# Optimization experiments

Hardware: AMD Instinct MI355X
Metric: run time of the kernel (lower is better)

The kernel has to match this reference:

```python
import jax, jax.numpy as jnp
import numpy as np

D_MODEL = 1024
NUM_HEADS = 16
HEAD_DIM = D_MODEL // NUM_HEADS


def setup_inputs() -> dict:
    key = jax.random.key(0)
    k_x, k_wqkv, k_bqkv, k_wo, k_bo = jax.random.split(key, 5)
    B, T = 2, 2048
    bound_qkv = 1.0 / np.sqrt(D_MODEL)
    bound_o = 1.0 / np.sqrt(D_MODEL)
    return {
        "x": jax.random.normal(k_x, (B, T, D_MODEL), dtype=jnp.float32),
        # stored as (in, out) for clean x @ W
        "w_qkv": jax.random.uniform(k_wqkv, (D_MODEL, 3 * D_MODEL), jnp.float32, -bound_qkv, bound_qkv),
        "b_qkv": jax.random.uniform(k_bqkv, (3 * D_MODEL,), jnp.float32, -bound_qkv, bound_qkv),
        "w_out": jax.random.uniform(k_wo, (D_MODEL, D_MODEL), jnp.float32, -bound_o, bound_o),
        "b_out": jax.random.uniform(k_bo, (D_MODEL,), jnp.float32, -bound_o, bound_o),
    }


def reference(x, w_qkv, b_qkv, w_out, b_out):
    B, T, C = x.shape
    H, Dh = NUM_HEADS, HEAD_DIM
    scale = jnp.sqrt(jnp.asarray(Dh, dtype=x.dtype))
    qkv = x @ w_qkv + b_qkv                      # [B, T, 3C]
    q, k, v = jnp.split(qkv, 3, axis=-1)         # each [B, T, C]
    # [B, T, C] -> [B, H, T, Dh]
    q = q.reshape(B, T, H, Dh).transpose(0, 2, 1, 3)
    k = k.reshape(B, T, H, Dh).transpose(0, 2, 1, 3)
    v = v.reshape(B, T, H, Dh).transpose(0, 2, 1, 3)
    scores = jnp.einsum("bhqd,bhkd->bhqk", q, k) / scale   # [B, H, T, T]
    probs = jax.nn.softmax(scores, axis=-1)
    attn = jnp.einsum("bhqk,bhkd->bhqd", probs, v)          # [B, H, T, Dh]
    attn = attn.transpose(0, 2, 1, 3).reshape(B, T, C)
    return attn @ w_out + b_out
```

## Files before the change

### kernel.cpp

```cpp
#include <hip/hip_runtime.h>
#include <stdint.h>

typedef __bf16 bf16x8 __attribute__((ext_vector_type(8)));
typedef float f32x4 __attribute__((ext_vector_type(4)));
typedef float f32x16 __attribute__((ext_vector_type(16)));
typedef unsigned short u16x8 __attribute__((ext_vector_type(8)));
typedef uint32_t u32x4 __attribute__((ext_vector_type(4)));

#define D_MODEL 1024
#define T_SEQ 2048
#define BATCH 2
#define NHEAD 16
#define HDIM 64
#define MROWS (BATCH * T_SEQ)
#define HEADS_TOTAL (BATCH * NHEAD)
#define QKV_ELEMS (HEADS_TOTAL * T_SEQ * HDIM)

#define QSCALE_LOG2 0.1803368801111204f

__device__ __forceinline__ unsigned short f32_to_bf16_rne(float f) {
    uint32_t u = __builtin_bit_cast(uint32_t, f);
    uint32_t r = (u + 0x7FFFu + ((u >> 16) & 1u)) >> 16;
    return (unsigned short)r;
}

__device__ __forceinline__ uint32_t pack2(float a, float b) {
    return (uint32_t)f32_to_bf16_rne(a) | ((uint32_t)f32_to_bf16_rne(b) << 16);
}

__device__ __forceinline__ void gload_lds16(const void* g, void* l) {
    __builtin_amdgcn_global_load_lds(
        (const __attribute__((address_space(1))) void*)g,
        (__attribute__((address_space(3))) void*)l, 16, 0, 0);
}

__device__ __forceinline__ f32x4 mfma_bf16(bf16x8 a, bf16x8 b, f32x4 c) {
    return __builtin_amdgcn_mfma_f32_16x16x32_bf16(a, b, c, 0, 0, 0);
}
__device__ __forceinline__ f32x16 mfma32(bf16x8 a, bf16x8 b, f32x16 c) {
    return __builtin_amdgcn_mfma_f32_32x32x16_bf16(a, b, c, 0, 0, 0);
}

__global__ void k_convert(const float4* __restrict__ in, u16x8* __restrict__ out, int n8) {
    int i = blockIdx.x * 256 + threadIdx.x;
    if (i >= n8) return;
    float4 a = in[i * 2];
    float4 b = in[i * 2 + 1];
    u16x8 r;
    r[0] = f32_to_bf16_rne(a.x); r[1] = f32_to_bf16_rne(a.y);
    r[2] = f32_to_bf16_rne(a.z); r[3] = f32_to_bf16_rne(a.w);
    r[4] = f32_to_bf16_rne(b.x); r[5] = f32_to_bf16_rne(b.y);
    r[6] = f32_to_bf16_rne(b.z); r[7] = f32_to_bf16_rne(b.w);
    out[i] = r;
}

__global__ void k_transpose_conv(const float* __restrict__ in, unsigned short* __restrict__ out,
                                 int R, int C) {
    __shared__ float tile[32][33];
    int nc = C >> 5;
    int tc0 = (blockIdx.x % nc) * 32;
    int tr0 = (blockIdx.x / nc) * 32;
    int tx = threadIdx.x & 31, ty = threadIdx.x >> 5;
#pragma unroll
    for (int i = 0; i < 4; ++i) {
        int r = ty * 4 + i;
        tile[r][tx] = in[(size_t)(tr0 + r) * C + tc0 + tx];
    }
    __syncthreads();
#pragma unroll
    for (int i = 0; i < 4; ++i) {
        int c = ty * 4 + i;
        out[(size_t)(tc0 + c) * R + tr0 + tx] = f32_to_bf16_rne(tile[tx][c]);
    }
}

template <int EPI>
__global__ __launch_bounds__(256) void k_gemm(const unsigned short* __restrict__ A,
                                              const unsigned short* __restrict__ Bt,
                                              const float* __restrict__ bias,
                                              void* __restrict__ outp,
                                              int M, int N, int K) {
    __shared__ __align__(16) unsigned short As[2][128 * 32];
    __shared__ __align__(16) unsigned short Bs[2][128 * 32];
    const int NB = N >> 7;
    int bm = blockIdx.x / NB, bn = blockIdx.x % NB;
    int tid = threadIdx.x;
    int lane = tid & 63, w = tid >> 6;
    int wr = w >> 1, wc = w & 1;
    int l15 = lane & 15, lg = lane >> 4;

    f32x4 acc[4][4] = {};

    const int nK = K >> 5;
    int c1 = tid, c2 = tid + 256;
    int r1 = c1 >> 2, o1 = (c1 & 3) * 8;
    int r2 = c2 >> 2, o2 = (c2 & 3) * 8;

#define GSTAGE(kt, buf)                                                          \
    do {                                                                         \
        int k0_ = (kt) * 32;                                                     \
        gload_lds16(A + (size_t)(bm * 128 + r1) * K + k0_ + o1,                  \
                    (char*)As[buf] + w * 1024);                                  \
        gload_lds16(A + (size_t)(bm * 128 + r2) * K + k0_ + o2,                  \
                    (char*)As[buf] + 4096 + w * 1024);                           \
        gload_lds16(Bt + (size_t)(bn * 128 + r1) * K + k0_ + o1,                 \
                    (char*)Bs[buf] + w * 1024);                                  \
        gload_lds16(Bt + (size_t)(bn * 128 + r2) * K + k0_ + o2,                 \
                    (char*)Bs[buf] + 4096 + w * 1024);                           \
    } while (0)

    GSTAGE(0, 0);
    __syncthreads();

    for (int kt = 0; kt < nK; ++kt) {
        int cur = kt & 1;
        if (kt + 1 < nK) GSTAGE(kt + 1, cur ^ 1);

        const unsigned short* Ac = As[cur];
        const unsigned short* Bc = Bs[cur];
        bf16x8 af[4], bfr[4];
#pragma unroll
        for (int i = 0; i < 4; ++i)
            af[i] = *(const bf16x8*)(Ac + (wr * 64 + i * 16 + l15) * 32 + lg * 8);
#pragma unroll
        for (int j = 0; j < 4; ++j)
            bfr[j] = *(const bf16x8*)(Bc + (wc * 64 + j * 16 + l15) * 32 + lg * 8);
#pragma unroll
        for (int i = 0; i < 4; ++i)
#pragma unroll
            for (int j = 0; j < 4; ++j)
                acc[i][j] = mfma_bf16(af[i], bfr[j], acc[i][j]);
        __syncthreads();
    }
#undef GSTAGE

    if (EPI == 1) {
        float* out = (float*)outp;
#pragma unroll
        for (int jn = 0; jn < 4; ++jn) {
            int n = bn * 128 + wc * 64 + jn * 16 + l15;
            float bv = bias[n];
#pragma unroll
            for (int i = 0; i < 4; ++i) {
#pragma unroll
                for (int j = 0; j < 4; ++j) {
                    int m = bm * 128 + wr * 64 + i * 16 + lg * 4 + j;
                    out[(size_t)m * N + n] = acc[i][jn][j] + bv;
                }
            }
        }
    } else {
        unsigned short* qkv = (unsigned short*)outp;
#pragma unroll
        for (int jn = 0; jn < 4; ++jn) {
            int n = bn * 128 + wc * 64 + jn * 16 + l15;
            float bv = bias[n];
            int part = n >> 10;
            int cc = n & 1023;
            int h = cc >> 6, d = cc & 63;
            float scale = (part == 0) ? QSCALE_LOG2 : 1.0f;
            unsigned short* dst = qkv + (size_t)part * QKV_ELEMS;
#pragma unroll
            for (int i = 0; i < 4; ++i) {
#pragma unroll
                for (int j = 0; j < 4; ++j) {
                    int m = bm * 128 + wr * 64 + i * 16 + lg * 4 + j;
                    int b = m >> 11, t = m & 2047;
                    float v = (acc[i][jn][j] + bv) * scale;
                    dst[((size_t)(b * NHEAD + h) * T_SEQ + t) * HDIM + d] = f32_to_bf16_rne(v);
                }
            }
        }
    }
}

__global__ void k_transpose_v(const unsigned short* __restrict__ V, unsigned short* __restrict__ Vt) {
    __shared__ unsigned short tile[64][66];
    int bh = blockIdx.x >> 5;
    int t0 = (blockIdx.x & 31) * 64;
    const unsigned short* Vb = V + (size_t)bh * T_SEQ * HDIM;
    unsigned short* Vtb = Vt + (size_t)bh * HDIM * T_SEQ;
    int d = threadIdx.x & 63, tq = threadIdx.x >> 6;
#pragma unroll
    for (int r = 0; r < 16; ++r) {
        int tl = tq * 16 + r;
        tile[tl][d] = Vb[(size_t)(t0 + tl) * HDIM + d];
    }
    __syncthreads();
    int tl = threadIdx.x & 63, dq = threadIdx.x >> 6;
#pragma unroll
    for (int r = 0; r < 16; ++r) {
        int dd = dq * 16 + r;
        Vtb[(size_t)dd * T_SEQ + t0 + tl] = tile[tl][dd];
    }
}

__global__ __launch_bounds__(256) void k_attn(const unsigned short* __restrict__ Qg,
                                              const unsigned short* __restrict__ Kg,
                                              const unsigned short* __restrict__ Vtg,
                                              unsigned short* __restrict__ Og) {
    __shared__ __align__(16) unsigned short Ks[2][64 * 64];
    __shared__ __align__(16) unsigned short Vs[2][64 * 64];

    const int NT = T_SEQ / 64;
    int bid = blockIdx.x;
    int idx = bid >> 3;
    int bh = (bid & 7) * 4 + (idx >> 4);
    int qt = idx & 15;
    int tid = threadIdx.x;
    int w = tid >> 6, lane = tid & 63;
    int l31 = lane & 31, hi = lane >> 5;
    int r7 = l31 & 7;

    const unsigned short* Qb = Qg + (size_t)bh * T_SEQ * HDIM;
    const unsigned short* Kb = Kg + (size_t)bh * T_SEQ * HDIM;
    const unsigned short* Vb = Vtg + (size_t)bh * HDIM * T_SEQ;

    int q0 = qt * 128 + w * 32;

    bf16x8 qf[4];
#pragma unroll
    for (int ks = 0; ks < 4; ++ks)
        qf[ks] = *(const bf16x8*)(Qb + (size_t)(q0 + l31) * HDIM + ks * 16 + hi * 8);

    f32x16 o_[2] = {};
    float m = -INFINITY, l = 0.f;

#define STAGE(tile, buf)                                                             \
    do {                                                                             \
        int kv0s = (tile) * 64;                                                      \
        _Pragma("unroll") for (int i_ = 0; i_ < 2; ++i_) {                           \
            int c_ = i_ * 256 + tid;                                                 \
            int row_ = c_ >> 3;                                                      \
            int cs_ = (c_ & 7) ^ (row_ & 7);                                         \
            gload_lds16(Kb + (size_t)(kv0s + row_) * HDIM + cs_ * 8,                 \
                        (char*)Ks[buf] + i_ * 4096 + w * 1024);                      \
            gload_lds16(Vb + (size_t)row_ * T_SEQ + kv0s + cs_ * 8,                  \
                        (char*)Vs[buf] + i_ * 4096 + w * 1024);                      \
        }                                                                            \
    } while (0)

    STAGE(0, 0);
    __syncthreads();

    for (int t = 0; t < NT; ++t) {
        int cur = t & 1;
        if (t + 1 < NT) STAGE(t + 1, cur ^ 1);

        const char* Kt = (const char*)Ks[cur];
        const char* Vt_ = (const char*)Vs[cur];

        f32x16 s_[2] = {};
#pragma unroll
        for (int ti = 0; ti < 2; ++ti) {
            int row = ti * 32 + l31;
#pragma unroll
            for (int ks = 0; ks < 4; ++ks) {
                bf16x8 kf = *(const bf16x8*)(Kt + row * 128 + ((((ks << 1) | hi) ^ r7) << 4));
                s_[ti] = mfma32(kf, qf[ks], s_[ti]);
            }
        }

        float t16[16];
#pragma unroll
        for (int rr = 0; rr < 16; ++rr) t16[rr] = fmaxf(s_[0][rr], s_[1][rr]);
#pragma unroll
        for (int st = 8; st >= 1; st >>= 1)
#pragma unroll
            for (int rr = 0; rr < 8; ++rr)
                if (rr < st) t16[rr] = fmaxf(t16[rr], t16[rr + st]);
        float mx = fmaxf(t16[0], __shfl_xor(t16[0], 32));

        if (__any(mx - m > 8.0f)) {
            float mn = fmaxf(m, mx);
            float sc = __builtin_exp2f(m - mn);
            m = mn;
            l *= sc;
#pragma unroll
            for (int rr = 0; rr < 16; ++rr) {
                o_[0][rr] *= sc;
                o_[1][rr] *= sc;
            }
        }

        float a16[16];
#pragma unroll
        for (int ti = 0; ti < 2; ++ti)
#pragma unroll
            for (int rr = 0; rr < 16; ++rr) s_[ti][rr] = __builtin_exp2f(s_[ti][rr] - m);
#pragma unroll
        for (int rr = 0; rr < 16; ++rr) a16[rr] = s_[0][rr] + s_[1][rr];
#pragma unroll
        for (int st = 8; st >= 1; st >>= 1)
#pragma unroll
            for (int rr = 0; rr < 8; ++rr)
                if (rr < st) a16[rr] += a16[rr + st];
        l += a16[0] + __shfl_xor(a16[0], 32);

        bf16x8 pa[4];
#pragma unroll
        for (int ks = 0; ks < 4; ++ks) {
            int ti = ks >> 1, k1 = ks & 1;
            uint32_t PA = pack2(s_[ti][8 * k1 + 0], s_[ti][8 * k1 + 1]);
            uint32_t PC = pack2(s_[ti][8 * k1 + 2], s_[ti][8 * k1 + 3]);
            uint32_t PB = pack2(s_[ti][8 * k1 + 4], s_[ti][8 * k1 + 5]);
            uint32_t PD = pack2(s_[ti][8 * k1 + 6], s_[ti][8 * k1 + 7]);
            uint32_t u0 = hi ? PA : PB;
            uint32_t u1 = hi ? PC : PD;
            uint32_t x0 = (uint32_t)__shfl_xor((int)u0, 32);
            uint32_t x1 = (uint32_t)__shfl_xor((int)u1, 32);
            u32x4 ww;
            ww[0] = hi ? x0 : PA;
            ww[1] = hi ? x1 : PC;
            ww[2] = hi ? PB : x0;
            ww[3] = hi ? PD : x1;
            pa[ks] = __builtin_bit_cast(bf16x8, ww);
        }

#pragma unroll
        for (int dn = 0; dn < 2; ++dn) {
            int row = dn * 32 + l31;
#pragma unroll
            for (int ks = 0; ks < 4; ++ks) {
                bf16x8 vf = *(const bf16x8*)(Vt_ + row * 128 + ((((ks << 1) | hi) ^ r7) << 4));
                o_[dn] = mfma32(vf, pa[ks], o_[dn]);
            }
        }
        __syncthreads();
    }
#undef STAGE

    float inv = 1.0f / l;
#pragma unroll
    for (int rr = 0; rr < 16; ++rr) {
        o_[0][rr] *= inv;
        o_[1][rr] *= inv;
    }
    char* eB = (char*)Ks + (size_t)w * 4096;
#pragma unroll
    for (int dn = 0; dn < 2; ++dn)
#pragma unroll
        for (int g = 0; g < 4; ++g) {
            uint32_t w0 = pack2(o_[dn][4 * g], o_[dn][4 * g + 1]);
            uint32_t w1 = pack2(o_[dn][4 * g + 2], o_[dn][4 * g + 3]);
            int c16 = (dn * 4 + g) ^ r7;
            *(uint2*)(eB + l31 * 128 + c16 * 16 + hi * 8) = make_uint2(w0, w1);
        }
    asm volatile("s_waitcnt lgkmcnt(0)" ::: "memory");
    int b = bh >> 4, h = bh & 15;
#pragma unroll
    for (int i = 0; i < 4; ++i) {
        int c = i * 64 + lane;
        int row = c >> 3;
        int c16l = c & 7;
        bf16x8 ov = *(const bf16x8*)(eB + row * 128 + ((c16l ^ (row & 7)) << 4));
        *(bf16x8*)(Og + ((size_t)(b * T_SEQ + q0 + row)) * D_MODEL + h * HDIM + c16l * 8) = ov;
    }
}

extern "C" void kernel_launch(void* const* d_in, const int* in_sizes, int n_in,
                              void* d_out, int out_size, void* d_ws, size_t ws_size,
                              hipStream_t stream) {
    const float* x = (const float*)d_in[0];
    const float* w_qkv = (const float*)d_in[1];
    const float* b_qkv = (const float*)d_in[2];
    const float* w_out = (const float*)d_in[3];
    const float* b_out = (const float*)d_in[4];
    float* out = (float*)d_out;
    char* ws = (char*)d_ws;

    unsigned short* x_bf   = (unsigned short*)(ws + 0);
    unsigned short* wqkv_t = (unsigned short*)(ws + 8388608);
    unsigned short* wout_t = (unsigned short*)(ws + 14680064);
    unsigned short* Qb     = (unsigned short*)(ws + 16777216);
    unsigned short* Kb     = (unsigned short*)(ws + 25165824);
    unsigned short* Vb     = (unsigned short*)(ws + 33554432);
    unsigned short* Vt     = x_bf;
    unsigned short* Ob     = Vb;

    k_convert<<<MROWS * D_MODEL / 8 / 256, 256, 0, stream>>>((const float4*)x, (u16x8*)x_bf,
                                                             MROWS * D_MODEL / 8);
    k_transpose_conv<<<(D_MODEL / 32) * (3 * D_MODEL / 32), 256, 0, stream>>>(w_qkv, wqkv_t,
                                                                              D_MODEL, 3 * D_MODEL);
    k_transpose_conv<<<(D_MODEL / 32) * (D_MODEL / 32), 256, 0, stream>>>(w_out, wout_t,
                                                                          D_MODEL, D_MODEL);
    k_gemm<0><<<(MROWS / 128) * (3 * D_MODEL / 128), 256, 0, stream>>>(x_bf, wqkv_t, b_qkv,
                                                                       (void*)Qb, MROWS,
                                                                       3 * D_MODEL, D_MODEL);
    k_transpose_v<<<HEADS_TOTAL * (T_SEQ / 64), 256, 0, stream>>>(Vb, Vt);
    k_attn<<<512, 256, 0, stream>>>(Qb, Kb, Vt, Ob);
    k_gemm<1><<<(MROWS / 128) * (D_MODEL / 128), 256, 0, stream>>>(Ob, wout_t, b_out, (void*)out,
                                                                   MROWS, D_MODEL, D_MODEL);
}
```

Before: 250.8 us.

## Shrink attention blocks to two waves, use hardware exp and MFMA priority hints

Attention blocks now hold two waves covering 64 queries, launched as 1024 blocks instead of 512, and the staging loop is rewritten with incremental pointers. Exponentials use the raw v_exp_f32 instruction, MFMA sections are wrapped in s_setprio, and the row-sum reduction is moved after the PV matmul to overlap with it. The aim is better occupancy and latency hiding, at the cost of each K/V tile being loaded by fewer waves, which raises global/L2 traffic per query.

```diff
diff --git a/kernel.cpp b/kernel.cpp
--- a/kernel.cpp
+++ b/kernel.cpp
@@ -26,6 +26,12 @@
 
 __device__ __forceinline__ uint32_t pack2(float a, float b) {
     return (uint32_t)f32_to_bf16_rne(a) | ((uint32_t)f32_to_bf16_rne(b) << 16);
+}
+
+__device__ __forceinline__ float exp2_hw(float x) {
+    float r;
+    asm("v_exp_f32 %0, %1" : "=v"(r) : "v"(x));
+    return r;
 }
 
 __device__ __forceinline__ void gload_lds16(const void* g, void* l) {
@@ -195,7 +201,7 @@
     }
 }
 
-__global__ __launch_bounds__(256) void k_attn(const unsigned short* __restrict__ Qg,
+__global__ __launch_bounds__(128) void k_attn(const unsigned short* __restrict__ Qg,
                                               const unsigned short* __restrict__ Kg,
                                               const unsigned short* __restrict__ Vtg,
                                               unsigned short* __restrict__ Og) {
@@ -205,8 +211,8 @@
     const int NT = T_SEQ / 64;
     int bid = blockIdx.x;
     int idx = bid >> 3;
-    int bh = (bid & 7) * 4 + (idx >> 4);
-    int qt = idx & 15;
+    int bh = (bid & 7) * 4 + (idx >> 5);
+    int qt = idx & 31;
     int tid = threadIdx.x;
     int w = tid >> 6, lane = tid & 63;
     int l31 = lane & 31, hi = lane >> 5;
@@ -216,7 +222,7 @@
     const unsigned short* Kb = Kg + (size_t)bh * T_SEQ * HDIM;
     const unsigned short* Vb = Vtg + (size_t)bh * HDIM * T_SEQ;
 
-    int q0 = qt * 128 + w * 32;
+    int q0 = qt * 64 + w * 32;
 
     bf16x8 qf[4];
 #pragma unroll
@@ -226,31 +232,33 @@
     f32x16 o_[2] = {};
     float m = -INFINITY, l = 0.f;
 
-#define STAGE(tile, buf)                                                             \
-    do {                                                                             \
-        int kv0s = (tile) * 64;                                                      \
-        _Pragma("unroll") for (int i_ = 0; i_ < 2; ++i_) {                           \
-            int c_ = i_ * 256 + tid;                                                 \
-            int row_ = c_ >> 3;                                                      \
-            int cs_ = (c_ & 7) ^ (row_ & 7);                                         \
-            gload_lds16(Kb + (size_t)(kv0s + row_) * HDIM + cs_ * 8,                 \
-                        (char*)Ks[buf] + i_ * 4096 + w * 1024);                      \
-            gload_lds16(Vb + (size_t)row_ * T_SEQ + kv0s + cs_ * 8,                  \
-                        (char*)Vs[buf] + i_ * 4096 + w * 1024);                      \
-        }                                                                            \
-    } while (0)
-
-    STAGE(0, 0);
+    int r0 = tid >> 3;
+    int cs = (tid & 7) ^ (r0 & 7);
+    const unsigned short* kp = Kb + r0 * HDIM + cs * 8;
+    const unsigned short* vp = Vb + (size_t)r0 * T_SEQ + cs * 8;
+
+    auto stage = [&](int buf) {
+#pragma unroll
+        for (int i_ = 0; i_ < 4; ++i_) {
+            gload_lds16(kp + i_ * (16 * HDIM), (char*)Ks[buf] + i_ * 2048 + w * 1024);
+            gload_lds16(vp + i_ * (16 * T_SEQ), (char*)Vs[buf] + i_ * 2048 + w * 1024);
+        }
+        kp += 64 * HDIM;
+        vp += 64;
+    };
+
+    stage(0);
     __syncthreads();
 
     for (int t = 0; t < NT; ++t) {
         int cur = t & 1;
-        if (t + 1 < NT) STAGE(t + 1, cur ^ 1);
+        if (t + 1 < NT) stage(cur ^ 1);
 
         const char* Kt = (const char*)Ks[cur];
         const char* Vt_ = (const char*)Vs[cur];
 
         f32x16 s_[2] = {};
+        __builtin_amdgcn_s_setprio(1);
 #pragma unroll
         for (int ti = 0; ti < 2; ++ti) {
             int row = ti * 32 + l31;
@@ -260,6 +268,7 @@
                 s_[ti] = mfma32(kf, qf[ks], s_[ti]);
             }
         }
+        __builtin_amdgcn_s_setprio(0);
 
         float t16[16];
 #pragma unroll
@@ -273,7 +282,7 @@
 
         if (__any(mx - m > 8.0f)) {
             float mn = fmaxf(m, mx);
-            float sc = __builtin_exp2f(m - mn);
+            float sc = exp2_hw(m - mn);
             m = mn;
             l *= sc;
 #pragma unroll
@@ -283,19 +292,10 @@
             }
         }
 
-        float a16[16];
 #pragma unroll
         for (int ti = 0; ti < 2; ++ti)
 #pragma unroll
-            for (int rr = 0; rr < 16; ++rr) s_[ti][rr] = __builtin_exp2f(s_[ti][rr] - m);
-#pragma unroll
-        for (int rr = 0; rr < 16; ++rr) a16[rr] = s_[0][rr] + s_[1][rr];
-#pragma unroll
-        for (int st = 8; st >= 1; st >>= 1)
-#pragma unroll
-            for (int rr = 0; rr < 8; ++rr)
-                if (rr < st) a16[rr] += a16[rr + st];
-        l += a16[0] + __shfl_xor(a16[0], 32);
+            for (int rr = 0; rr < 16; ++rr) s_[ti][rr] = exp2_hw(s_[ti][rr] - m);
 
         bf16x8 pa[4];
 #pragma unroll
@@ -317,6 +317,7 @@
             pa[ks] = __builtin_bit_cast(bf16x8, ww);
         }
 
+        __builtin_amdgcn_s_setprio(1);
 #pragma unroll
         for (int dn = 0; dn < 2; ++dn) {
             int row = dn * 32 + l31;
@@ -326,9 +327,20 @@
                 o_[dn] = mfma32(vf, pa[ks], o_[dn]);
             }
         }
+        __builtin_amdgcn_s_setprio(0);
+
+        float a16[16];
+#pragma unroll
+        for (int rr = 0; rr < 16; ++rr) a16[rr] = s_[0][rr] + s_[1][rr];
+#pragma unroll
+        for (int st = 8; st >= 1; st >>= 1)
+#pragma unroll
+            for (int rr = 0; rr < 8; ++rr)
+                if (rr < st) a16[rr] += a16[rr + st];
+        l += a16[0] + __shfl_xor(a16[0], 32);
+
         __syncthreads();
     }
-#undef STAGE
 
     float inv = 1.0f / l;
 #pragma unroll
@@ -388,7 +400,7 @@
                                                                        (void*)Qb, MROWS,
                                                                        3 * D_MODEL, D_MODEL);
     k_transpose_v<<<HEADS_TOTAL * (T_SEQ / 64), 256, 0, stream>>>(Vb, Vt);
-    k_attn<<<512, 256, 0, stream>>>(Qb, Kb, Vt, Ob);
+    k_attn<<<1024, 128, 0, stream>>>(Qb, Kb, Vt, Ob);
     k_gemm<1><<<(MROWS / 128) * (D_MODEL / 128), 256, 0, stream>>>(Ob, wout_t, b_out, (void*)out,
                                                                    MROWS, D_MODEL, D_MODEL);
 }
```

New measurement: 238.5 us. 1.05x faster.
